# Kernel tuning notes

Hardware: AMD Instinct MI355X
Metric: run time of the kernel (lower is better)

## Reference

```python
import jax, jax.numpy as jnp
import numpy as np

BBOX_STD = np.array([0.1, 0.1, 0.2, 0.2], np.float32)
MIN_CONF = 0.7
MAX_INST = 100
NMS_THR = 0.3


def setup_inputs() -> dict:
    key = jax.random.key(0)
    k1, k2, k3 = jax.random.split(key, 3)
    B, N, C = 8, 1000, 81
    # rois: valid normalized boxes (y1<=y2, x1<=x2)
    pts = jax.random.uniform(k1, (B, N, 2, 2), dtype=jnp.float32)
    lo = jnp.min(pts, axis=2)   # [B,N,2] -> (y1,x1)
    hi = jnp.max(pts, axis=2)   # [B,N,2] -> (y2,x2)
    rois = jnp.concatenate([lo, hi], axis=-1)
    # confident softmax class probabilities
    logits = 5.0 * jax.random.normal(k2, (B, N, C), dtype=jnp.float32)
    mrcnn_class = jax.nn.softmax(logits, axis=-1)
    mrcnn_bbox = 0.2 * jax.random.normal(k3, (B, N, C, 4), dtype=jnp.float32)
    # image_meta: [id(1), orig_shape(3), image_shape(3), window(4), scale(1), active_class_ids(81)]
    meta = np.zeros((B, 1 + 3 + 3 + 4 + 1 + C), np.float32)
    meta[:, 1:4] = [1024.0, 1024.0, 3.0]
    meta[:, 4:7] = [1024.0, 1024.0, 3.0]
    meta[:, 7:11] = [0.0, 0.0, 1024.0, 1024.0]
    meta[:, 11] = 1.0
    return {"rois": rois, "mrcnn_class": mrcnn_class,
            "mrcnn_bbox": mrcnn_bbox, "image_meta": jnp.asarray(meta)}


def _apply_box_deltas(boxes, deltas):
    # boxes/deltas: [N,4] (y1,x1,y2,x2) / (dy,dx,log dh,log dw)
    h = boxes[:, 2] - boxes[:, 0]
    w = boxes[:, 3] - boxes[:, 1]
    cy = boxes[:, 0] + 0.5 * h
    cx = boxes[:, 1] + 0.5 * w
    cy = cy + deltas[:, 0] * h
    cx = cx + deltas[:, 1] * w
    h = h * jnp.exp(deltas[:, 2])
    w = w * jnp.exp(deltas[:, 3])
    return jnp.stack([cy - 0.5 * h, cx - 0.5 * w, cy + 0.5 * h, cx + 0.5 * w], axis=1)


def _clip_boxes(boxes, window):
    wy1, wx1, wy2, wx2 = window[0], window[1], window[2], window[3]
    y1 = jnp.clip(boxes[:, 0], wy1, wy2)
    x1 = jnp.clip(boxes[:, 1], wx1, wx2)
    y2 = jnp.clip(boxes[:, 2], wy1, wy2)
    x2 = jnp.clip(boxes[:, 3], wx1, wx2)
    return jnp.stack([y1, x1, y2, x2], axis=1)


def _iou_matrix(boxes):
    # boxes: [N,4] -> pairwise IoU [N,N]
    y1, x1, y2, x2 = boxes[:, 0], boxes[:, 1], boxes[:, 2], boxes[:, 3]
    area = (y2 - y1) * (x2 - x1)
    iy1 = jnp.maximum(y1[:, None], y1[None, :])
    ix1 = jnp.maximum(x1[:, None], x1[None, :])
    iy2 = jnp.minimum(y2[:, None], y2[None, :])
    ix2 = jnp.minimum(x2[:, None], x2[None, :])
    inter = jnp.maximum(iy2 - iy1, 0.0) * jnp.maximum(ix2 - ix1, 0.0)
    union = area[:, None] + area[None, :] - inter
    return inter / jnp.maximum(union, 1e-10)


def _refine_one_image(rois, probs, deltas, window):
    N = rois.shape[0]
    idx = jnp.arange(N)
    class_ids = jnp.argmax(probs, axis=1)                 # [N]
    class_scores = probs[idx, class_ids]                  # [N]
    deltas_spec = deltas[idx, class_ids] * jnp.asarray(BBOX_STD)
    refined = _clip_boxes(_apply_box_deltas(rois, deltas_spec), window)
    # filter: background and low-confidence
    valid = (class_ids > 0) & (class_scores >= MIN_CONF)
    scores = jnp.where(valid, class_scores, -1.0)
    # sort by score desc, greedy class-aware NMS (== per-class NMS merged)
    order = jnp.argsort(-scores)
    boxes_s = refined[order]
    scores_s = scores[order]
    cls_s = class_ids[order]
    iou = _iou_matrix(boxes_s)                            # [N,N]
    suppress = (iou > NMS_THR) & (cls_s[:, None] == cls_s[None, :])
    keep0 = scores_s > -0.5

    def body(i, keep):
        sup = suppress[i] & keep[i] & (jnp.arange(N) > i)
        return keep & (~sup)

    keep = jax.lax.fori_loop(0, N, body, keep0)
    final_scores = jnp.where(keep, scores_s, -1.0)
    top_scores, top_idx = jax.lax.top_k(final_scores, MAX_INST)
    ok = top_scores > -0.5                                # [MAX_INST]
    out_boxes = jnp.where(ok[:, None], boxes_s[top_idx], 0.0)
    out_cls = jnp.where(ok, cls_s[top_idx].astype(jnp.float32), 0.0)
    out_scr = jnp.where(ok, top_scores, 0.0)
    return jnp.concatenate([out_boxes, out_cls[:, None], out_scr[:, None]], axis=1)


def reference(rois, mrcnn_class, mrcnn_bbox, image_meta):
    # parse image meta: image_shape = meta[:,4:7], window (pixels) = meta[:,7:11]
    image_shape = image_meta[0, 4:7]
    h, w = image_shape[0], image_shape[1]
    scale = jnp.stack([h, w, h, w]) - 1.0
    shift = jnp.array([0.0, 0.0, 1.0, 1.0], jnp.float32)
    window = (image_meta[:, 7:11] - shift) / scale        # [B,4] normalized
    dets = jax.vmap(_refine_one_image)(rois, mrcnn_class, mrcnn_bbox, window)
    return dets  # [B, MAX_INST, 6]
```

## Files before the change

kernel.cpp:

```cpp
#include <hip/hip_runtime.h>


#define NROI 1000
#define NCLS 81
#define MAXI 100
#define PAD  1024
#define BLK  1024
#define NW   (BLK / 64)
#define MIN_CONF 0.7f
#define NMS_THR  0.3f

typedef float f32x4u __attribute__((ext_vector_type(4), aligned(4)));
typedef unsigned long long u64;

__device__ __forceinline__ u64 shfl_xor_u64(u64 v, int m) {
  unsigned lo = (unsigned)__shfl_xor((int)(unsigned)(v & 0xFFFFFFFFull), m, 64);
  unsigned hi = (unsigned)__shfl_xor((int)(unsigned)(v >> 32), m, 64);
  return (((u64)hi) << 32) | lo;
}

__global__ __launch_bounds__(64) void refine_kernel(
    const float* __restrict__ rois,
    const float* __restrict__ probs,
    const float* __restrict__ deltas,
    const float* __restrict__ meta,
    float4* __restrict__ ws_box,
    float2* __restrict__ ws_aux,
    int meta_stride)
{
  const int b   = blockIdx.x >> 4;
  const int roi = ((blockIdx.x & 15) << 6) + threadIdx.x;
  if (roi >= NROI) return;

  const float* p = probs + ((size_t)b * NROI + roi) * NCLS;
  float best = p[0];
  int   bc = 0;
  for (int c0 = 1; c0 < NCLS; c0 += 4) {
    f32x4u v = *(const f32x4u*)(p + c0);
#pragma unroll
    for (int e = 0; e < 4; ++e) {
      float f = v[e];
      if (f > best) { best = f; bc = c0 + e; }
    }
  }

  const float4 dd = *(const float4*)(deltas + (((size_t)b * NROI + roi) * NCLS + bc) * 4);
  const float4 rr = *(const float4*)(rois + ((size_t)b * NROI + roi) * 4);

  float hh = rr.z - rr.x, ww = rr.w - rr.y;
  float cy = rr.x + 0.5f * hh + (dd.x * 0.1f) * hh;
  float cx = rr.y + 0.5f * ww + (dd.y * 0.1f) * ww;
  hh *= expf(dd.z * 0.2f);
  ww *= expf(dd.w * 0.2f);
  float ny1 = cy - 0.5f * hh, nx1 = cx - 0.5f * ww;
  float ny2 = cy + 0.5f * hh, nx2 = cx + 0.5f * ww;

  float H = meta[4], W = meta[5];
  float sy = H - 1.0f, sx = W - 1.0f;
  const float* m = meta + (size_t)b * meta_stride;
  float wy1 = m[7] / sy, wx1 = m[8] / sx;
  float wy2 = (m[9] - 1.0f) / sy, wx2 = (m[10] - 1.0f) / sx;

  float4 bb;
  bb.x = fminf(fmaxf(ny1, wy1), wy2);
  bb.y = fminf(fmaxf(nx1, wx1), wx2);
  bb.z = fminf(fmaxf(ny2, wy1), wy2);
  bb.w = fminf(fmaxf(nx2, wx1), wx2);

  bool valid = (bc > 0) && (best >= MIN_CONF);
  float score = valid ? best : -1.0f;

  ws_box[(size_t)b * PAD + roi] = bb;
  ws_aux[(size_t)b * PAD + roi] = make_float2(score, (float)bc);
}

__global__ __launch_bounds__(BLK) void sortnms_kernel(
    const float4* __restrict__ ws_box,
    const float2* __restrict__ ws_aux,
    float* __restrict__ out)
{
  const int b    = blockIdx.x;
  const int tid  = threadIdx.x;
  const int lane = tid & 63;
  const int wv   = tid >> 6;

  __shared__ u64    skeyA[BLK], skeyB[BLK];
  __shared__ float4 u_box[NROI];
  __shared__ float4 sbox[NROI];
  __shared__ u64    cmask[NW][NCLS];
  __shared__ u64    s_alive[NW];
  __shared__ int    wcnt[NW];

  for (int k = tid; k < MAXI * 6; k += BLK)
    out[(size_t)b * (MAXI * 6) + k] = 0.0f;

  float sc = -1.0f;
  int   cls = 0;
  if (tid < NROI) {
    float2 a = ws_aux[(size_t)b * PAD + tid];
    sc  = a.x;
    cls = (int)a.y;
    u_box[tid] = ws_box[(size_t)b * PAD + tid];
  }
  const bool valid = sc > -0.5f;

  u64 vb = __ballot(valid);
  if (lane == 0) wcnt[wv] = (int)__popcll(vb);
  __syncthreads();
  int V = 0, cbase0 = 0;
  for (int w = 0; w < NW; ++w) {
    int c = wcnt[w];
    if (w < wv) cbase0 += c;
    V += c;
  }
  if (valid) {
    int slot = cbase0 + (int)__popcll(vb & ((1ull << (unsigned)lane) - 1ull));
    unsigned bits = __float_as_uint(sc);
    unsigned ord  = bits | 0x80000000u;
    skeyA[slot] = (((u64)(~ord)) << 32) | ((unsigned)tid << 7) | (unsigned)cls;
  }
  if (tid >= V) skeyA[tid] = 0xFFFFFFFFFFFFFFFFull;
  {
    u64* cf = &cmask[0][0];
    for (int i = tid; i < NW * NCLS; i += BLK) cf[i] = 0ull;
  }
  __syncthreads();

  int P = 64;
  while (P < V) P <<= 1;
  const bool insort = tid < P;

  u64 key = skeyA[tid];
  int ldst = 1;
  for (int k = 2; k <= P; k <<= 1) {
    for (int j = k >> 1; j > 0; j >>= 1) {
      const bool takeMin = (((tid & j) == 0) == ((tid & k) == 0));
      if (j >= 64) {
        u64* buf = (ldst & 1) ? skeyB : skeyA;
        if (insort) buf[tid] = key;
        __syncthreads();
        if (insort) {
          u64 other = buf[tid ^ j];
          key = (takeMin ? (other < key) : (other > key)) ? other : key;
        }
        ++ldst;
      } else if (insort) {
        u64 other = shfl_xor_u64(key, j);
        key = (takeMin ? (other < key) : (other > key)) ? other : key;
      }
    }
  }

  bool   mykeep = tid < V;
  float4 jb = make_float4(0.f, 0.f, 0.f, 0.f);
  float  jarea = 0.f;
  int    jcls = -1;
  if (mykeep) {
    int oid = (int)((key >> 7) & 0x3FFull);
    jcls = (int)(key & 0x7Full);
    jb = u_box[oid];
    jarea = (jb.z - jb.x) * (jb.w - jb.y);
    sbox[tid] = jb;
    atomicOr(&cmask[wv][jcls], 1ull << (unsigned)lane);
  }
  __syncthreads();

  int kc = 0;
  const int nchunks = (V + 63) >> 6;
  for (int c = 0; c < nchunks; ++c) {
    const int cb = c << 6;

    u64 jsup = 0ull;
    if (mykeep && wv >= c) {
      u64 m = cmask[c][jcls];
      if (wv == c) m &= (1ull << (unsigned)lane) - 1ull;
      while (m) {
        int l = __ffsll((long long)m) - 1;
        m &= m - 1;
        float4 lb = sbox[cb + l];
        float la = (lb.z - lb.x) * (lb.w - lb.y);
        float iy1 = fmaxf(lb.x, jb.x), ix1 = fmaxf(lb.y, jb.y);
        float iy2 = fminf(lb.z, jb.z), ix2 = fminf(lb.w, jb.w);
        float inter = fmaxf(iy2 - iy1, 0.f) * fmaxf(ix2 - ix1, 0.f);
        if (inter > NMS_THR * fmaxf(la + jarea - inter, 1e-10f))
          jsup |= (1ull << (unsigned)l);
      }
    }

    if (wv == c) {
      u64 aliveW = __ballot(mykeep);
      u64 rem = aliveW;
      while (rem) {
        int l = __ffsll((long long)rem) - 1;
        rem &= ~(1ull << (unsigned)l);
        u64 kill = __ballot((int)((jsup >> (unsigned)l) & 1ull));
        aliveW &= ~kill;
        rem    &= ~kill;
      }
      mykeep = ((aliveW >> (unsigned)lane) & 1ull) != 0;
      if (lane == 0) s_alive[c] = aliveW;
    }
    __syncthreads();
    const u64 alive = s_alive[c];
    if (wv > c && (jsup & alive)) mykeep = false;
    kc += (int)__popcll(alive);
    if (kc >= MAXI) break;
  }

  u64 bm = __ballot((int)mykeep);
  if (lane == 0) wcnt[wv] = (int)__popcll(bm);
  __syncthreads();
  if (mykeep) {
    int base2 = 0;
    for (int q = 0; q < wv; ++q) base2 += wcnt[q];
    int slot = base2 + (int)__popcll(bm & ((1ull << (unsigned)lane) - 1ull));
    if (slot < MAXI) {
      unsigned ordhi = ~(unsigned)(key >> 32);
      float score = __uint_as_float(ordhi & 0x7FFFFFFFu);
      float* o = out + ((size_t)b * MAXI + slot) * 6;
      o[0] = jb.x; o[1] = jb.y; o[2] = jb.z; o[3] = jb.w;
      o[4] = (float)jcls;
      o[5] = score;
    }
  }
}

extern "C" void kernel_launch(void* const* d_in, const int* in_sizes, int n_in,
                              void* d_out, int out_size, void* d_ws, size_t ws_size,
                              hipStream_t stream) {
  const float* rois   = (const float*)d_in[0];
  const float* probs  = (const float*)d_in[1];
  const float* deltas = (const float*)d_in[2];
  const float* meta   = (const float*)d_in[3];
  float* out = (float*)d_out;

  const int nb = in_sizes[0] / (NROI * 4);
  const int meta_stride = in_sizes[3] / nb;

  float4* ws_box = (float4*)d_ws;
  float2* ws_aux = (float2*)((char*)d_ws + (size_t)nb * PAD * sizeof(float4));

  refine_kernel<<<nb * 16, 64, 0, stream>>>(rois, probs, deltas, meta,
                                            ws_box, ws_aux, meta_stride);
  sortnms_kernel<<<nb, BLK, 0, stream>>>(ws_box, ws_aux, out);
}
```

Before: 27.07 us.

## Fuse box refinement into sort/NMS kernel to drop second launch

Merges the per-ROI argmax/box-refine kernel into the per-image sort+NMS kernel, so each 1024-thread block computes its own ROIs' class, score and clipped box directly into shared memory. This removes a kernel launch and the global workspace write/read between stages. In exchange, the refine phase runs on only one block per image instead of 16 small blocks per image, reducing parallelism for the probability reads.

After: 27.94 us. 1.03x slower.

```diff
diff --git a/kernel.cpp b/kernel.cpp
--- a/kernel.cpp
+++ b/kernel.cpp
@@ -4,7 +4,6 @@
 #define NROI 1000
 #define NCLS 81
 #define MAXI 100
-#define PAD  1024
 #define BLK  1024
 #define NW   (BLK / 64)
 #define MIN_CONF 0.7f
@@ -19,65 +18,13 @@
   return (((u64)hi) << 32) | lo;
 }
 
-__global__ __launch_bounds__(64) void refine_kernel(
+__global__ __launch_bounds__(BLK) void detection_kernel(
     const float* __restrict__ rois,
     const float* __restrict__ probs,
     const float* __restrict__ deltas,
     const float* __restrict__ meta,
-    float4* __restrict__ ws_box,
-    float2* __restrict__ ws_aux,
+    float* __restrict__ out,
     int meta_stride)
-{
-  const int b   = blockIdx.x >> 4;
-  const int roi = ((blockIdx.x & 15) << 6) + threadIdx.x;
-  if (roi >= NROI) return;
-
-  const float* p = probs + ((size_t)b * NROI + roi) * NCLS;
-  float best = p[0];
-  int   bc = 0;
-  for (int c0 = 1; c0 < NCLS; c0 += 4) {
-    f32x4u v = *(const f32x4u*)(p + c0);
-#pragma unroll
-    for (int e = 0; e < 4; ++e) {
-      float f = v[e];
-      if (f > best) { best = f; bc = c0 + e; }
-    }
-  }
-
-  const float4 dd = *(const float4*)(deltas + (((size_t)b * NROI + roi) * NCLS + bc) * 4);
-  const float4 rr = *(const float4*)(rois + ((size_t)b * NROI + roi) * 4);
-
-  float hh = rr.z - rr.x, ww = rr.w - rr.y;
-  float cy = rr.x + 0.5f * hh + (dd.x * 0.1f) * hh;
-  float cx = rr.y + 0.5f * ww + (dd.y * 0.1f) * ww;
-  hh *= expf(dd.z * 0.2f);
-  ww *= expf(dd.w * 0.2f);
-  float ny1 = cy - 0.5f * hh, nx1 = cx - 0.5f * ww;
-  float ny2 = cy + 0.5f * hh, nx2 = cx + 0.5f * ww;
-
-  float H = meta[4], W = meta[5];
-  float sy = H - 1.0f, sx = W - 1.0f;
-  const float* m = meta + (size_t)b * meta_stride;
-  float wy1 = m[7] / sy, wx1 = m[8] / sx;
-  float wy2 = (m[9] - 1.0f) / sy, wx2 = (m[10] - 1.0f) / sx;
-
-  float4 bb;
-  bb.x = fminf(fmaxf(ny1, wy1), wy2);
-  bb.y = fminf(fmaxf(nx1, wx1), wx2);
-  bb.z = fminf(fmaxf(ny2, wy1), wy2);
-  bb.w = fminf(fmaxf(nx2, wx1), wx2);
-
-  bool valid = (bc > 0) && (best >= MIN_CONF);
-  float score = valid ? best : -1.0f;
-
-  ws_box[(size_t)b * PAD + roi] = bb;
-  ws_aux[(size_t)b * PAD + roi] = make_float2(score, (float)bc);
-}
-
-__global__ __launch_bounds__(BLK) void sortnms_kernel(
-    const float4* __restrict__ ws_box,
-    const float2* __restrict__ ws_aux,
-    float* __restrict__ out)
 {
   const int b    = blockIdx.x;
   const int tid  = threadIdx.x;
@@ -97,10 +44,45 @@
   float sc = -1.0f;
   int   cls = 0;
   if (tid < NROI) {
-    float2 a = ws_aux[(size_t)b * PAD + tid];
-    sc  = a.x;
-    cls = (int)a.y;
-    u_box[tid] = ws_box[(size_t)b * PAD + tid];
+    const float* p = probs + ((size_t)b * NROI + tid) * NCLS;
+    float best = p[0];
+    int   bc = 0;
+    for (int c0 = 1; c0 < NCLS; c0 += 4) {
+      f32x4u v = *(const f32x4u*)(p + c0);
+#pragma unroll
+      for (int e = 0; e < 4; ++e) {
+        float f = v[e];
+        if (f > best) { best = f; bc = c0 + e; }
+      }
+    }
+
+    const float4 dd = *(const float4*)(deltas + (((size_t)b * NROI + tid) * NCLS + bc) * 4);
+    const float4 rr = *(const float4*)(rois + ((size_t)b * NROI + tid) * 4);
+
+    float hh = rr.z - rr.x, ww = rr.w - rr.y;
+    float cy = rr.x + 0.5f * hh + (dd.x * 0.1f) * hh;
+    float cx = rr.y + 0.5f * ww + (dd.y * 0.1f) * ww;
+    hh *= expf(dd.z * 0.2f);
+    ww *= expf(dd.w * 0.2f);
+    float ny1 = cy - 0.5f * hh, nx1 = cx - 0.5f * ww;
+    float ny2 = cy + 0.5f * hh, nx2 = cx + 0.5f * ww;
+
+    float H = meta[4], W = meta[5];
+    float sy = H - 1.0f, sx = W - 1.0f;
+    const float* m = meta + (size_t)b * meta_stride;
+    float wy1 = m[7] / sy, wx1 = m[8] / sx;
+    float wy2 = (m[9] - 1.0f) / sy, wx2 = (m[10] - 1.0f) / sx;
+
+    float4 bb;
+    bb.x = fminf(fmaxf(ny1, wy1), wy2);
+    bb.y = fminf(fmaxf(nx1, wx1), wx2);
+    bb.z = fminf(fmaxf(ny2, wy1), wy2);
+    bb.w = fminf(fmaxf(nx2, wx1), wx2);
+    u_box[tid] = bb;
+
+    cls = bc;
+    bool valid = (bc > 0) && (best >= MIN_CONF);
+    sc = valid ? best : -1.0f;
   }
   const bool valid = sc > -0.5f;
 
@@ -115,8 +97,7 @@
   }
   if (valid) {
     int slot = cbase0 + (int)__popcll(vb & ((1ull << (unsigned)lane) - 1ull));
-    unsigned bits = __float_as_uint(sc);
-    unsigned ord  = bits | 0x80000000u;
+    unsigned ord = __float_as_uint(sc) | 0x80000000u;
     skeyA[slot] = (((u64)(~ord)) << 32) | ((unsigned)tid << 7) | (unsigned)cls;
   }
   if (tid >= V) skeyA[tid] = 0xFFFFFFFFFFFFFFFFull;
@@ -237,10 +218,6 @@
   const int nb = in_sizes[0] / (NROI * 4);
   const int meta_stride = in_sizes[3] / nb;
 
-  float4* ws_box = (float4*)d_ws;
-  float2* ws_aux = (float2*)((char*)d_ws + (size_t)nb * PAD * sizeof(float4));
-
-  refine_kernel<<<nb * 16, 64, 0, stream>>>(rois, probs, deltas, meta,
-                                            ws_box, ws_aux, meta_stride);
-  sortnms_kernel<<<nb, BLK, 0, stream>>>(ws_box, ws_aux, out);
+  detection_kernel<<<nb, BLK, 0, stream>>>(rois, probs, deltas, meta, out,
+                                           meta_stride);
 }
```
